# Kernel optimization log

Measured on AMD Instinct MI355X. Metric: run time of the kernel, lower is better.

The kernel has to match this reference:

```python
import jax, jax.numpy as jnp
import numpy as np

B, S, H = 8, 2048, 1024
NH, HD, NS, K = 16, 64, 64, 4  # num_heads, head_dim, state_size, conv kernel


def setup_inputs() -> dict:
    key = jax.random.key(0)
    ks = jax.random.split(key, 16)
    sc = 0.02
    return {
        "x": jax.random.normal(ks[0], (B, S, H), dtype=jnp.float32),
        # weights stored (in, out) so y = x @ W + b
        "in_proj_w": jax.random.normal(ks[1], (H, 2 * H), dtype=jnp.float32) * sc,
        "conv_w": jax.random.normal(ks[2], (H, 1, K), dtype=jnp.float32) * sc,
        "conv_b": jnp.zeros((H,), dtype=jnp.float32),
        "bb_w": jax.random.normal(ks[3], (HD, HD), dtype=jnp.float32) * sc,
        "bb_b": jnp.zeros((HD,), dtype=jnp.float32),
        "f1_w": jax.random.normal(ks[4], (HD, NS), dtype=jnp.float32) * sc,
        "f1_b": jnp.zeros((NS,), dtype=jnp.float32),
        "f2_w": jax.random.normal(ks[5], (HD, NS), dtype=jnp.float32) * sc,
        "f2_b": jnp.zeros((NS,), dtype=jnp.float32),
        "tau_a_w": jax.random.normal(ks[6], (HD, NS), dtype=jnp.float32) * sc,
        "tau_a_b": jnp.zeros((NS,), dtype=jnp.float32),
        "tau_b": jnp.zeros((NS,), dtype=jnp.float32),
        "decay_w": jax.random.normal(ks[7], (HD, NS), dtype=jnp.float32) * sc,
        "decay_b": jnp.zeros((NS,), dtype=jnp.float32),
        "state_out_w": jax.random.normal(ks[8], (NS, HD), dtype=jnp.float32) * sc,
        "state_out_b": jnp.zeros((HD,), dtype=jnp.float32),
        "out_proj_w": jax.random.normal(ks[9], (H, H), dtype=jnp.float32) * sc,
    }


def _short_conv(x, w, b):
    # x: (B,S,D) depthwise causal conv, kernel K, left-pad K-1
    xc = jnp.transpose(x, (0, 2, 1))  # (B,D,S)
    y = jax.lax.conv_general_dilated(
        xc, w, window_strides=(1,), padding=[(K - 1, 0)],
        feature_group_count=H, dimension_numbers=("NCH", "OIH", "NCH"))
    y = y + b[None, :, None]
    return jnp.transpose(y, (0, 2, 1))  # (B,S,D)


def _scan(decay, candidate):
    # decay, candidate: (B,S,NH,NS); h_t = d_t*h_{t-1} + (1-d_t)*c_t
    d = jnp.transpose(decay, (1, 0, 2, 3))      # (S,B,NH,NS)
    c = jnp.transpose(candidate, (1, 0, 2, 3))

    def step(h, dc):
        dt, ct = dc
        h = dt * h + (1.0 - dt) * ct
        return h, h

    h0 = jnp.zeros(d.shape[1:], dtype=decay.dtype)
    _, hs = jax.lax.scan(step, h0, (d, c))
    return jnp.transpose(hs, (1, 0, 2, 3))      # (B,S,NH,NS)


def reference(x, in_proj_w, conv_w, conv_b, bb_w, bb_b, f1_w, f1_b,
              f2_w, f2_b, tau_a_w, tau_a_b, tau_b, decay_w, decay_b,
              state_out_w, state_out_b, out_proj_w):
    xz = x @ in_proj_w                       # (B,S,2H)
    x_path, z_gate = jnp.split(xz, 2, axis=-1)
    x_path = jax.nn.silu(_short_conv(x_path, conv_w, conv_b))
    x_heads = x_path.reshape(B, S, NH, HD)
    bb = jax.nn.silu(x_heads @ bb_w + bb_b)  # backbone (1 layer)
    f1 = jnp.tanh(bb @ f1_w + f1_b)
    f2 = jnp.tanh(bb @ f2_w + f2_b)
    tau = jax.nn.sigmoid(bb @ tau_a_w + tau_a_b + tau_b)
    candidate = f1 * (1.0 - tau) + f2 * tau
    decay = jax.nn.sigmoid(bb @ decay_w + decay_b)
    h_seq = _scan(decay, candidate)          # (B,S,NH,NS)
    out = h_seq @ state_out_w + state_out_b  # (B,S,NH,HD)
    out = out.reshape(B, S, H)
    out = out * jax.nn.silu(z_gate)
    return out @ out_proj_w
```

## Files before the change

### kernel.cpp

```cpp
#include <hip/hip_runtime.h>
#include <hip/hip_bf16.h>
#include <math.h>

#define BN   8
#define SN   2048
#define HN   1024
#define NTOK 16384
#define NHD  16
#define HDD  64
#define NSD  64

typedef __attribute__((ext_vector_type(8))) short short8;
typedef __attribute__((ext_vector_type(4))) float f32x4;

__device__ __forceinline__ float fsig(float x)  { return 1.f / (1.f + __expf(-x)); }
__device__ __forceinline__ float fsilu(float x) { return x / (1.f + __expf(-x)); }
__device__ __forceinline__ float ftanh(float x) {
    const float t = __expf(-2.f * fabsf(x));
    const float r = (1.f - t) / (1.f + t);
    return x >= 0.f ? r : -r;
}
__device__ __forceinline__ unsigned pack_cd(float cand, float dec) {
    __hip_bfloat16 cb_ = __float2bfloat16(cand);
    __hip_bfloat16 db_ = __float2bfloat16(dec);
    return (unsigned)*(unsigned short*)&cb_ | ((unsigned)*(unsigned short*)&db_ << 16);
}
__device__ __forceinline__ void gload_lds16(const void* g, void* l) {
    __builtin_amdgcn_global_load_lds(
        (const __attribute__((address_space(1))) unsigned int*)g,
        (__attribute__((address_space(3))) unsigned int*)l, 16, 0, 0);
}

__global__ __launch_bounds__(256)
void x_to_a_bf(const float* __restrict__ X, __hip_bfloat16* __restrict__ A)
{
    const int idx = blockIdx.x * 256 + threadIdx.x;
    const int r = idx >> 7;
    const int c = idx & 127;
    const float* src = &X[(size_t)r * 1024 + c * 8];
    alignas(16) __hip_bfloat16 b[8];
#pragma unroll
    for (int j = 0; j < 8; ++j) b[j] = __float2bfloat16(src[j]);
    const int cs = (c & 120) | ((c & 7) ^ (r & 7));
    *(short8*)&A[(size_t)r * 1024 + cs * 8] = *(const short8*)b;
}

__global__ __launch_bounds__(256)
void w_to_bt_bf(const float* __restrict__ W, __hip_bfloat16* __restrict__ BT, int N)
{
    __shared__ float t[64][65];
    const int k0 = blockIdx.x * 64;
    const int n0 = blockIdx.y * 64;
    const int c  = threadIdx.x & 63, r4 = threadIdx.x >> 6;
#pragma unroll
    for (int rr = 0; rr < 64; rr += 4)
        t[rr + r4][c] = W[(size_t)(k0 + rr + r4) * N + n0 + c];
    __syncthreads();
#pragma unroll
    for (int oo = 0; oo < 2; ++oo) {
        const int o = r4 * 2 + oo;
        alignas(16) __hip_bfloat16 b[8];
#pragma unroll
        for (int j = 0; j < 8; ++j)
            b[j] = __float2bfloat16(t[o * 8 + j][c]);
        const int n = n0 + c;
        const int cglob = (k0 >> 3) + o;
        const int cs = (cglob & 120) | ((cglob & 7) ^ (n & 7));
        *(short8*)&BT[(size_t)n * 1024 + cs * 8] = *(const short8*)b;
    }
}

__global__ __launch_bounds__(256)
void w5_to_wt(const float* __restrict__ w0, const float* __restrict__ w1,
              const float* __restrict__ w2, const float* __restrict__ w3,
              const float* __restrict__ w4, __hip_bfloat16* __restrict__ WT5)
{
    const int idx = blockIdx.x * 256 + threadIdx.x;
    if (idx >= 2560) return;
    const int o = idx & 7, n = (idx >> 3) & 63, mat = idx >> 9;
    const float* W = mat == 0 ? w0 : mat == 1 ? w1 : mat == 2 ? w2 : mat == 3 ? w3 : w4;
    alignas(16) __hip_bfloat16 b[8];
#pragma unroll
    for (int j = 0; j < 8; ++j)
        b[j] = __float2bfloat16(W[(o * 8 + j) * 64 + n]);
    *(short8*)&WT5[(size_t)(mat * 64 + n) * 64 + ((o ^ (n & 7)) * 8)] = *(const short8*)b;
}

template<int NCT, int MODE>
__global__ __launch_bounds__(512, 2)
void mfma_gemm256(const __hip_bfloat16* __restrict__ A,
                  const __hip_bfloat16* __restrict__ BT,
                  float* __restrict__ out0, float* __restrict__ out1)
{
    __shared__ __hip_bfloat16 lds[2][2][16384];
    const int tid  = threadIdx.x;
    const int lane = tid & 63, wave = tid >> 6;
    const int wr   = wave >> 2, wc = wave & 3;
    const int l15  = lane & 15, l4 = lane >> 4;

    const int nwg = gridDim.x;
    const int cpx = nwg >> 3;
    const int swz = (blockIdx.x & 7) * cpx + (blockIdx.x >> 3);
    const int mt = swz / NCT, nt = swz % NCT;
    const int row0 = mt * 256, col0 = nt * 256;

    const int s_c = tid & 7;
    const int s_r = (tid >> 3) & 63;

    f32x4 acc[8][4];
#pragma unroll
    for (int m = 0; m < 8; ++m)
#pragma unroll
        for (int n = 0; n < 4; ++n) acc[m][n] = (f32x4)0.f;

#define STAGE_I(I, TT, BUF)                                                    \
    {                                                                          \
        const int mat_ = (I) >> 2;                                             \
        const int row_ = ((I) & 3) * 64 + s_r;                                 \
        const __hip_bfloat16* src_ = (mat_ == 0)                               \
            ? &A [(size_t)(row0 + row_) * 1024 + ((TT) << 6) + s_c * 8]        \
            : &BT[(size_t)(col0 + row_) * 1024 + ((TT) << 6) + s_c * 8];       \
        gload_lds16(src_, &lds[BUF][mat_][row_ * 64 + s_c * 8]);               \
    }

#pragma unroll
    for (int i = 0; i < 8; ++i) STAGE_I(i, 0, 0)
    __syncthreads();

    for (int t = 0; t < 16; ++t) {
        const int cur = t & 1, nxt = cur ^ 1;
        const bool pf = (t < 15);

#pragma unroll
        for (int ks = 0; ks < 2; ++ks) {
            if (pf) {
#pragma unroll
                for (int i = ks * 4; i < ks * 4 + 4; ++i) STAGE_I(i, t + 1, nxt)
            }

            short8 af[8], bf[4];
#pragma unroll
            for (int m = 0; m < 8; ++m) {
                const int row = wr * 128 + m * 16 + l15;
                const int ch = (ks * 4 + l4) ^ (l15 & 7);
                af[m] = *(const short8*)&lds[cur][0][row * 64 + ch * 8];
            }
#pragma unroll
            for (int n = 0; n < 4; ++n) {
                const int row = wc * 64 + n * 16 + l15;
                const int ch = (ks * 4 + l4) ^ (l15 & 7);
                bf[n] = *(const short8*)&lds[cur][1][row * 64 + ch * 8];
            }

            __builtin_amdgcn_s_setprio(1);
#pragma unroll
            for (int m = 0; m < 8; ++m)
#pragma unroll
                for (int n = 0; n < 4; ++n)
                    acc[m][n] = __builtin_amdgcn_mfma_f32_16x16x32_bf16(af[m], bf[n], acc[m][n], 0, 0, 0);
            __builtin_amdgcn_s_setprio(0);
        }
        __syncthreads();
    }
#undef STAGE_I

    const int orow = l4 * 4, ocol = l15;
#pragma unroll
    for (int M = 0; M < 8; ++M)
#pragma unroll
        for (int N = 0; N < 4; ++N) {
            const int c = col0 + wc * 64 + N * 16 + ocol;
#pragma unroll
            for (int q = 0; q < 4; ++q) {
                const int r = row0 + wr * 128 + M * 16 + orow + q;
                const float v = acc[M][N][q];
                if (MODE == 0) {
                    out0[(size_t)r * (NCT * 256) + c] = v;
                } else {
                    if (c < 1024) out0[(size_t)r * 1024 + c] = v;
                    else          out1[(size_t)r * 1024 + (c - 1024)] = fsilu(v);
                }
            }
        }
}

__global__ __launch_bounds__(256)
void conv_silu_bf(const float* __restrict__ xp, const float* __restrict__ cw,
                  const float* __restrict__ cb, __hip_bfloat16* __restrict__ Xbf)
{
    const int idx = blockIdx.x * 256 + threadIdx.x;
    const int g  = idx & 127;
    const int bt = idx >> 7;
    const int t  = bt & (SN - 1);
    const int c0 = g * 8;

    float acc[8];
#pragma unroll
    for (int j = 0; j < 8; ++j) acc[j] = cb[c0 + j];
    float4 cwv[8];
#pragma unroll
    for (int j = 0; j < 8; ++j) cwv[j] = *(const float4*)&cw[(c0 + j) * 4];
    const float* cwf = (const float*)cwv;

#pragma unroll
    for (int k = 0; k < 4; ++k) {
        if (t - 3 + k >= 0) {
            const float* xr = xp + (((size_t)(bt - 3 + k)) << 10) + c0;
            const float4 u0 = *(const float4*)&xr[0];
            const float4 u1 = *(const float4*)&xr[4];
            const float u[8] = {u0.x, u0.y, u0.z, u0.w, u1.x, u1.y, u1.z, u1.w};
#pragma unroll
            for (int j = 0; j < 8; ++j) acc[j] += cwf[j * 4 + k] * u[j];
        }
    }

    alignas(16) __hip_bfloat16 b[8];
#pragma unroll
    for (int j = 0; j < 8; ++j) b[j] = __float2bfloat16(fsilu(acc[j]));

    const int head = g >> 3;
    const int o    = g & 7;
    const size_t row = (size_t)bt * 16 + head;
    *(short8*)&Xbf[row * 64 + ((o ^ (head & 7)) * 8)] = *(const short8*)b;
}

__global__ __launch_bounds__(512, 4)
void backbone_mfma(const __hip_bfloat16* __restrict__ Xbf,
                   const __hip_bfloat16* __restrict__ WT5,
                   const float* __restrict__ bbb,
                   const float* __restrict__ f1b, const float* __restrict__ f2b,
                   const float* __restrict__ taub, const float* __restrict__ taub2,
                   const float* __restrict__ decb,
                   unsigned* __restrict__ cd)
{
    __shared__ __hip_bfloat16 Wl[5 * 64 * 64];
    __shared__ __hip_bfloat16 Bb[128 * 64];
    const int tid  = threadIdx.x;
    const int lane = tid & 63, wave = tid >> 6;
    const int l15  = lane & 15, l4 = lane >> 4;
    const int e7   = l15 & 7;

#pragma unroll
    for (int r = 0; r < 5; ++r) {
        const int blk = r * 8 + wave;
        gload_lds16(WT5 + blk * 512 + lane * 8, Wl + blk * 512);
    }

    const __hip_bfloat16* xrow = Xbf + ((size_t)(blockIdx.x * 8 + wave) * 16) * 64;
    short8 xa[2];
#pragma unroll
    for (int s = 0; s < 2; ++s)
        xa[s] = *(const short8*)&xrow[l15 * 64 + (((s * 4 + l4) ^ e7) * 8)];

    __syncthreads();

#pragma unroll
    for (int nt = 0; nt < 4; ++nt) {
        short8 wb[2];
#pragma unroll
        for (int s = 0; s < 2; ++s)
            wb[s] = *(const short8*)&Wl[(nt * 16 + l15) * 64 + (((s * 4 + l4) ^ e7) * 8)];
        f32x4 ac = (f32x4)0.f;
        ac = __builtin_amdgcn_mfma_f32_16x16x32_bf16(xa[0], wb[0], ac, 0, 0, 0);
        ac = __builtin_amdgcn_mfma_f32_16x16x32_bf16(xa[1], wb[1], ac, 0, 0, 0);
        const int col = nt * 16 + l15;
        const float bc = bbb[col];
#pragma unroll
        for (int q = 0; q < 4; ++q) {
            const int r15 = l4 * 4 + q;
            Bb[(wave * 16 + r15) * 64 + ((col >> 3) ^ (r15 & 7)) * 8 + (col & 7)] =
                __float2bfloat16(fsilu(ac[q] + bc));
        }
    }

    short8 ba[2];
#pragma unroll
    for (int s = 0; s < 2; ++s)
        ba[s] = *(const short8*)&Bb[(wave * 16 + l15) * 64 + (((s * 4 + l4) ^ e7) * 8)];

#pragma unroll
    for (int nt = 0; nt < 4; ++nt) {
        f32x4 a2[4];
#pragma unroll
        for (int m = 0; m < 4; ++m) a2[m] = (f32x4)0.f;

#pragma unroll
        for (int mat = 0; mat < 4; ++mat) {
            short8 w2[2];
#pragma unroll
            for (int s = 0; s < 2; ++s)
                w2[s] = *(const short8*)&Wl[((mat + 1) * 64 + nt * 16 + l15) * 64 + (((s * 4 + l4) ^ e7) * 8)];
            a2[mat] = __builtin_amdgcn_mfma_f32_16x16x32_bf16(ba[0], w2[0], a2[mat], 0, 0, 0);
            a2[mat] = __builtin_amdgcn_mfma_f32_16x16x32_bf16(ba[1], w2[1], a2[mat], 0, 0, 0);
        }

        const int col = nt * 16 + l15;
        const float b1 = f1b[col], b2 = f2b[col];
        const float b3 = taub[col] + taub2[col], b4 = decb[col];
        const size_t Rbase = (size_t)blockIdx.x * 128 + wave * 16;
#pragma unroll
        for (int q = 0; q < 4; ++q) {
            const size_t R = Rbase + l4 * 4 + q;
            const float f1v = ftanh(a2[0][q] + b1);
            const float f2v = ftanh(a2[1][q] + b2);
            const float tv  = fsig (a2[2][q] + b3);
            const float dv  = fsig (a2[3][q] + b4);
            cd[R * 64 + col] = pack_cd(f1v * (1.f - tv) + f2v * tv, dv);
        }
    }
}

__global__ __launch_bounds__(256)
void scan_compose(const unsigned* __restrict__ cd,
                  float* __restrict__ Ach, float* __restrict__ Bch)
{
    const int idx = blockIdx.x * 256 + threadIdx.x;
    const int p  = idx & 1023;
    const int rest = idx >> 10;
    const int ch = rest & 63, b = rest >> 6;
    float A = 1.f, Bv = 0.f;
    const size_t base = ((size_t)(b * SN + ch * 32) << 10) + p;
    for (int t = 0; t < 32; ++t) {
        const unsigned u = cd[base + ((size_t)t << 10)];
        const float c = __uint_as_float(u << 16);
        const float d = __uint_as_float(u & 0xffff0000u);
        A  *= d;
        Bv  = d * Bv + (1.f - d) * c;
    }
    Ach[(ch << 13) + (b << 10) + p] = A;
    Bch[(ch << 13) + (b << 10) + p] = Bv;
}

__global__ __launch_bounds__(256)
void scan_chunks(const float* __restrict__ Ach, const float* __restrict__ Bch,
                 float* __restrict__ hstart)
{
    const int q = blockIdx.x * 256 + threadIdx.x;
    float h = 0.f;
    for (int ch = 0; ch < 64; ++ch) {
        hstart[(ch << 13) + q] = h;
        h = Ach[(ch << 13) + q] * h + Bch[(ch << 13) + q];
    }
}

__global__ __launch_bounds__(256)
void scan_apply(const unsigned* __restrict__ cd,
                const float* __restrict__ hstart, __hip_bfloat16* __restrict__ Hhl)
{
    const int idx = blockIdx.x * 256 + threadIdx.x;
    const int p  = idx & 1023;
    const int rest = idx >> 10;
    const int ch = rest & 63, b = rest >> 6;
    const int nh = p >> 6, ns = p & 63;
    const int hpos = ((ns >> 3) ^ (nh & 7)) * 8 + (ns & 7);
    float h = hstart[(ch << 13) + (b << 10) + p];
    const int t0 = b * SN + ch * 32;
    const size_t base = ((size_t)t0 << 10) + p;
    for (int t = 0; t < 32; ++t) {
        const unsigned u = cd[base + ((size_t)t << 10)];
        const float c = __uint_as_float(u << 16);
        const float d = __uint_as_float(u & 0xffff0000u);
        h = d * h + (1.f - d) * c;
        Hhl[((size_t)(t0 + t) * 16 + nh) * 64 + hpos] = __float2bfloat16(h);
    }
}

__global__ __launch_bounds__(256, 4)
void stateout_mfma(const __hip_bfloat16* __restrict__ Hhl,
                   const float* __restrict__ sow, const float* __restrict__ sob,
                   const float* __restrict__ zs, __hip_bfloat16* __restrict__ gA)
{
    __shared__ __hip_bfloat16 Wl[64 * 64];
    __shared__ __hip_bfloat16 Hl[128 * 64];
    const int tid  = threadIdx.x;
    const int lane = tid & 63, wave = tid >> 6;
    const int l15  = lane & 15, l4 = lane >> 4;
    const int e7   = l15 & 7;

    {
        const int n = tid & 63;
        const int o0 = tid >> 6;
#pragma unroll
        for (int oo = 0; oo < 2; ++oo) {
            const int o = o0 + oo * 4;
            alignas(16) __hip_bfloat16 b[8];
#pragma unroll
            for (int j = 0; j < 8; ++j)
                b[j] = __float2bfloat16(sow[(o * 8 + j) * 64 + n]);
            *(short8*)&Wl[n * 64 + ((o ^ (n & 7)) * 8)] = *(const short8*)b;
        }
    }
    const __hip_bfloat16* hsrc = Hhl + (size_t)blockIdx.x * 8192;
#pragma unroll
    for (int r = 0; r < 4; ++r) {
        const int blk = r * 4 + wave;
        gload_lds16(hsrc + blk * 512 + lane * 8, Hl + blk * 512);
    }
    __syncthreads();

    short8 ha[2][2];
#pragma unroll
    for (int mt2 = 0; mt2 < 2; ++mt2)
#pragma unroll
        for (int s = 0; s < 2; ++s)
            ha[mt2][s] = *(const short8*)&Hl[(wave * 32 + mt2 * 16 + l15) * 64 + (((s * 4 + l4) ^ e7) * 8)];

#pragma unroll
    for (int nt = 0; nt < 4; ++nt) {
        short8 wb[2];
#pragma unroll
        for (int s = 0; s < 2; ++s)
            wb[s] = *(const short8*)&Wl[(nt * 16 + l15) * 64 + (((s * 4 + l4) ^ e7) * 8)];
        f32x4 ac[2] = {(f32x4)0.f, (f32x4)0.f};
#pragma unroll
        for (int mt2 = 0; mt2 < 2; ++mt2) {
            ac[mt2] = __builtin_amdgcn_mfma_f32_16x16x32_bf16(ha[mt2][0], wb[0], ac[mt2], 0, 0, 0);
            ac[mt2] = __builtin_amdgcn_mfma_f32_16x16x32_bf16(ha[mt2][1], wb[1], ac[mt2], 0, 0, 0);
        }
        const int col = nt * 16 + l15;
        const float bj = sob[col];
#pragma unroll
        for (int mt2 = 0; mt2 < 2; ++mt2)
#pragma unroll
            for (int q = 0; q < 4; ++q) {
                const size_t th = (size_t)blockIdx.x * 128 + wave * 32 + mt2 * 16 + l4 * 4 + q;
                const float v = (ac[mt2][q] + bj) * zs[th * 64 + col];
                const size_t token = th >> 4;
                const int colg = (int)(th & 15) * 64 + col;
                const int cg = colg >> 3, jg = colg & 7;
                const int cs = (cg & 120) | ((cg & 7) ^ ((int)(token & 7)));
                gA[token * 1024 + cs * 8 + jg] = __float2bfloat16(v);
            }
    }
}

extern "C" void kernel_launch(void* const* d_in, const int* in_sizes, int n_in,
                              void* d_out, int out_size, void* d_ws, size_t ws_size,
                              hipStream_t stream)
{
    const float* x     = (const float*)d_in[0];
    const float* ipw   = (const float*)d_in[1];
    const float* cw    = (const float*)d_in[2];
    const float* cb    = (const float*)d_in[3];
    const float* bbw   = (const float*)d_in[4];
    const float* bbb   = (const float*)d_in[5];
    const float* f1w   = (const float*)d_in[6];
    const float* f1b   = (const float*)d_in[7];
    const float* f2w   = (const float*)d_in[8];
    const float* f2b   = (const float*)d_in[9];
    const float* tauw  = (const float*)d_in[10];
    const float* taub  = (const float*)d_in[11];
    const float* taub2 = (const float*)d_in[12];
    const float* decw  = (const float*)d_in[13];
    const float* decb  = (const float*)d_in[14];
    const float* sow   = (const float*)d_in[15];
    const float* sob   = (const float*)d_in[16];
    const float* opw   = (const float*)d_in[17];

    float* out = (float*)d_out;
    char*  ws  = (char*)d_ws;
    const size_t MB = 1024 * 1024;

    __hip_bfloat16* Abf   = (__hip_bfloat16*)(ws);
    __hip_bfloat16* Xbf   = (__hip_bfloat16*)(ws);
    __hip_bfloat16* Hhl   = (__hip_bfloat16*)(ws + 32 * MB);
    float*          xpath = (float*)(ws + 64 * MB);
    __hip_bfloat16* gA    = (__hip_bfloat16*)(ws + 64 * MB);
    __hip_bfloat16* BTin  = (__hip_bfloat16*)(ws + 128 * MB);
    unsigned*       cd    = (unsigned*)(ws + 128 * MB);
    __hip_bfloat16* WT5   = (__hip_bfloat16*)(ws + 192 * MB);
    float*          Ach   = (float*)(ws + 192 * MB);
    float*          Bch   = Ach + 524288;
    float*          hst   = Bch + 524288;
    __hip_bfloat16* BTout = (__hip_bfloat16*)(ws + 192 * MB);
    float*          zsilu = out;

    x_to_a_bf<<<8192, 256, 0, stream>>>(x, Abf);
    w_to_bt_bf<<<dim3(16, 32), 256, 0, stream>>>(ipw, BTin, 2048);
    w5_to_wt<<<10, 256, 0, stream>>>(bbw, f1w, f2w, tauw, decw, WT5);
    mfma_gemm256<8, 1><<<512, 512, 0, stream>>>(Abf, BTin, xpath, zsilu);
    conv_silu_bf<<<8192, 256, 0, stream>>>(xpath, cw, cb, Xbf);
    backbone_mfma<<<2048, 512, 0, stream>>>(Xbf, WT5, bbb, f1b, f2b,
                                            taub, taub2, decb, cd);
    scan_compose<<<2048, 256, 0, stream>>>(cd, Ach, Bch);
    scan_chunks<<<32, 256, 0, stream>>>(Ach, Bch, hst);
    scan_apply<<<2048, 256, 0, stream>>>(cd, hst, Hhl);
    w_to_bt_bf<<<dim3(16, 16), 256, 0, stream>>>(opw, BTout, 1024);
    stateout_mfma<<<2048, 256, 0, stream>>>(Hhl, sow, sob, zsilu, gA);
    mfma_gemm256<4, 0><<<256, 512, 0, stream>>>(gA, BTout, out, nullptr);
}
```

Measured before the change: 320.8 us.

## Shrink GEMM tiles to 128x256 with BK=32 and emit bf16 intermediates

Reworks the MFMA GEMM to use 128x256 output tiles with a 32-wide K step, a smaller LDS footprint and a 4-block occupancy hint, doubling the grid. The swizzle pattern in the A/B staging kernels and in stateout changes from 8-chunk to 4-chunk XOR to match. The input projection now writes x_path and silu(z) as bf16 instead of fp32, and the conv and stateout kernels read bf16. The goal is more occupancy and less intermediate memory traffic, at the cost of lower per-tile reuse, more barriers per K, and reduced precision in the intermediates.

```diff
diff --git a/kernel.cpp b/kernel.cpp
--- a/kernel.cpp
+++ b/kernel.cpp
@@ -25,6 +25,9 @@
     __hip_bfloat16 db_ = __float2bfloat16(dec);
     return (unsigned)*(unsigned short*)&cb_ | ((unsigned)*(unsigned short*)&db_ << 16);
 }
+__device__ __forceinline__ float bf2f(unsigned short u) {
+    return __uint_as_float((unsigned)u << 16);
+}
 __device__ __forceinline__ void gload_lds16(const void* g, void* l) {
     __builtin_amdgcn_global_load_lds(
         (const __attribute__((address_space(1))) unsigned int*)g,
@@ -41,7 +44,7 @@
     alignas(16) __hip_bfloat16 b[8];
 #pragma unroll
     for (int j = 0; j < 8; ++j) b[j] = __float2bfloat16(src[j]);
-    const int cs = (c & 120) | ((c & 7) ^ (r & 7));
+    const int cs = (c & ~3) | ((c & 3) ^ (r & 3));
     *(short8*)&A[(size_t)r * 1024 + cs * 8] = *(const short8*)b;
 }
 
@@ -65,7 +68,7 @@
             b[j] = __float2bfloat16(t[o * 8 + j][c]);
         const int n = n0 + c;
         const int cglob = (k0 >> 3) + o;
-        const int cs = (cglob & 120) | ((cglob & 7) ^ (n & 7));
+        const int cs = (cglob & ~3) | ((cglob & 3) ^ (n & 3));
         *(short8*)&BT[(size_t)n * 1024 + cs * 8] = *(const short8*)b;
     }
 }
@@ -87,12 +90,13 @@
 }
 
 template<int NCT, int MODE>
-__global__ __launch_bounds__(512, 2)
-void mfma_gemm256(const __hip_bfloat16* __restrict__ A,
-                  const __hip_bfloat16* __restrict__ BT,
-                  float* __restrict__ out0, float* __restrict__ out1)
-{
-    __shared__ __hip_bfloat16 lds[2][2][16384];
+__global__ __launch_bounds__(512, 4)
+void mfma_gemm(const __hip_bfloat16* __restrict__ A,
+               const __hip_bfloat16* __restrict__ BT,
+               float* __restrict__ outf,
+               __hip_bfloat16* __restrict__ xb, __hip_bfloat16* __restrict__ zb)
+{
+    __shared__ __hip_bfloat16 lds[2][12288];
     const int tid  = threadIdx.x;
     const int lane = tid & 63, wave = tid >> 6;
     const int wr   = wave >> 2, wc = wave & 3;
@@ -102,90 +106,83 @@
     const int cpx = nwg >> 3;
     const int swz = (blockIdx.x & 7) * cpx + (blockIdx.x >> 3);
     const int mt = swz / NCT, nt = swz % NCT;
-    const int row0 = mt * 256, col0 = nt * 256;
-
-    const int s_c = tid & 7;
-    const int s_r = (tid >> 3) & 63;
-
-    f32x4 acc[8][4];
-#pragma unroll
-    for (int m = 0; m < 8; ++m)
+    const int row0 = mt * 128, col0 = nt * 256;
+
+    const int s_c = tid & 3;
+    const int s_r = tid >> 2;
+
+    f32x4 acc[4][4];
+#pragma unroll
+    for (int m = 0; m < 4; ++m)
 #pragma unroll
         for (int n = 0; n < 4; ++n) acc[m][n] = (f32x4)0.f;
 
-#define STAGE_I(I, TT, BUF)                                                    \
+    const int rdch = (0 ^ 0);
+
+#define STAGE(TT, BUF)                                                         \
     {                                                                          \
-        const int mat_ = (I) >> 2;                                             \
-        const int row_ = ((I) & 3) * 64 + s_r;                                 \
-        const __hip_bfloat16* src_ = (mat_ == 0)                               \
-            ? &A [(size_t)(row0 + row_) * 1024 + ((TT) << 6) + s_c * 8]        \
-            : &BT[(size_t)(col0 + row_) * 1024 + ((TT) << 6) + s_c * 8];       \
-        gload_lds16(src_, &lds[BUF][mat_][row_ * 64 + s_c * 8]);               \
-    }
-
-#pragma unroll
-    for (int i = 0; i < 8; ++i) STAGE_I(i, 0, 0)
+        const int kk_ = (TT) << 5;                                             \
+        gload_lds16(&A[(size_t)(row0 + s_r) * 1024 + kk_ + s_c * 8],           \
+                    &lds[BUF][s_r * 32 + s_c * 8]);                            \
+        _Pragma("unroll")                                                      \
+        for (int h_ = 0; h_ < 2; ++h_) {                                       \
+            const int r_ = h_ * 128 + s_r;                                     \
+            gload_lds16(&BT[(size_t)(col0 + r_) * 1024 + kk_ + s_c * 8],       \
+                        &lds[BUF][4096 + r_ * 32 + s_c * 8]);                  \
+        }                                                                      \
+    }
+
+    STAGE(0, 0)
     __syncthreads();
 
-    for (int t = 0; t < 16; ++t) {
+    for (int t = 0; t < 32; ++t) {
         const int cur = t & 1, nxt = cur ^ 1;
-        const bool pf = (t < 15);
-
-#pragma unroll
-        for (int ks = 0; ks < 2; ++ks) {
-            if (pf) {
-#pragma unroll
-                for (int i = ks * 4; i < ks * 4 + 4; ++i) STAGE_I(i, t + 1, nxt)
-            }
-
-            short8 af[8], bf[4];
-#pragma unroll
-            for (int m = 0; m < 8; ++m) {
-                const int row = wr * 128 + m * 16 + l15;
-                const int ch = (ks * 4 + l4) ^ (l15 & 7);
-                af[m] = *(const short8*)&lds[cur][0][row * 64 + ch * 8];
-            }
-#pragma unroll
-            for (int n = 0; n < 4; ++n) {
-                const int row = wc * 64 + n * 16 + l15;
-                const int ch = (ks * 4 + l4) ^ (l15 & 7);
-                bf[n] = *(const short8*)&lds[cur][1][row * 64 + ch * 8];
-            }
-
-            __builtin_amdgcn_s_setprio(1);
-#pragma unroll
-            for (int m = 0; m < 8; ++m)
-#pragma unroll
-                for (int n = 0; n < 4; ++n)
-                    acc[m][n] = __builtin_amdgcn_mfma_f32_16x16x32_bf16(af[m], bf[n], acc[m][n], 0, 0, 0);
-            __builtin_amdgcn_s_setprio(0);
-        }
+        if (t < 31) STAGE(t + 1, nxt)
+
+        const int ch = (l4 ^ (l15 & 3)) * 8;
+        short8 af[4], bf[4];
+#pragma unroll
+        for (int m = 0; m < 4; ++m)
+            af[m] = *(const short8*)&lds[cur][(wr * 64 + m * 16 + l15) * 32 + ch];
+#pragma unroll
+        for (int n = 0; n < 4; ++n)
+            bf[n] = *(const short8*)&lds[cur][4096 + (wc * 64 + n * 16 + l15) * 32 + ch];
+
+        __builtin_amdgcn_s_setprio(1);
+#pragma unroll
+        for (int m = 0; m < 4; ++m)
+#pragma unroll
+            for (int n = 0; n < 4; ++n)
+                acc[m][n] = __builtin_amdgcn_mfma_f32_16x16x32_bf16(af[m], bf[n], acc[m][n], 0, 0, 0);
+        __builtin_amdgcn_s_setprio(0);
+
         __syncthreads();
     }
-#undef STAGE_I
+#undef STAGE
 
     const int orow = l4 * 4, ocol = l15;
 #pragma unroll
-    for (int M = 0; M < 8; ++M)
-#pragma unroll
-        for (int N = 0; N < 4; ++N) {
-            const int c = col0 + wc * 64 + N * 16 + ocol;
+    for (int m = 0; m < 4; ++m)
+#pragma unroll
+        for (int n = 0; n < 4; ++n) {
+            const int c = col0 + wc * 64 + n * 16 + ocol;
 #pragma unroll
             for (int q = 0; q < 4; ++q) {
-                const int r = row0 + wr * 128 + M * 16 + orow + q;
-                const float v = acc[M][N][q];
+                const int r = row0 + wr * 64 + m * 16 + orow + q;
+                const float v = acc[m][n][q];
                 if (MODE == 0) {
-                    out0[(size_t)r * (NCT * 256) + c] = v;
+                    outf[(size_t)r * (NCT * 256) + c] = v;
                 } else {
-                    if (c < 1024) out0[(size_t)r * 1024 + c] = v;
-                    else          out1[(size_t)r * 1024 + (c - 1024)] = fsilu(v);
+                    if (c < 1024) xb[(size_t)r * 1024 + c] = __float2bfloat16(v);
+                    else          zb[(size_t)r * 1024 + (c - 1024)] = __float2bfloat16(fsilu(v));
                 }
             }
         }
-}
-
-__global__ __launch_bounds__(256)
-void conv_silu_bf(const float* __restrict__ xp, const float* __restrict__ cw,
+    (void)rdch;
+}
+
+__global__ __launch_bounds__(256)
+void conv_silu_bf(const __hip_bfloat16* __restrict__ xp, const float* __restrict__ cw,
                   const float* __restrict__ cb, __hip_bfloat16* __restrict__ Xbf)
 {
     const int idx = blockIdx.x * 256 + threadIdx.x;
@@ -205,12 +202,10 @@
 #pragma unroll
     for (int k = 0; k < 4; ++k) {
         if (t - 3 + k >= 0) {
-            const float* xr = xp + (((size_t)(bt - 3 + k)) << 10) + c0;
-            const float4 u0 = *(const float4*)&xr[0];
-            const float4 u1 = *(const float4*)&xr[4];
-            const float u[8] = {u0.x, u0.y, u0.z, u0.w, u1.x, u1.y, u1.z, u1.w};
-#pragma unroll
-            for (int j = 0; j < 8; ++j) acc[j] += cwf[j * 4 + k] * u[j];
+            const short8 u = *(const short8*)&xp[(((size_t)(bt - 3 + k)) << 10) + c0];
+#pragma unroll
+            for (int j = 0; j < 8; ++j)
+                acc[j] += cwf[j * 4 + k] * bf2f((unsigned short)u[j]);
         }
     }
 
@@ -368,7 +363,7 @@
 __global__ __launch_bounds__(256, 4)
 void stateout_mfma(const __hip_bfloat16* __restrict__ Hhl,
                    const float* __restrict__ sow, const float* __restrict__ sob,
-                   const float* __restrict__ zs, __hip_bfloat16* __restrict__ gA)
+                   const __hip_bfloat16* __restrict__ zs, __hip_bfloat16* __restrict__ gA)
 {
     __shared__ __hip_bfloat16 Wl[64 * 64];
     __shared__ __hip_bfloat16 Hl[128 * 64];
@@ -424,11 +419,12 @@
 #pragma unroll
             for (int q = 0; q < 4; ++q) {
                 const size_t th = (size_t)blockIdx.x * 128 + wave * 32 + mt2 * 16 + l4 * 4 + q;
-                const float v = (ac[mt2][q] + bj) * zs[th * 64 + col];
+                const float z = bf2f(*(const unsigned short*)&zs[th * 64 + col]);
+                const float v = (ac[mt2][q] + bj) * z;
                 const size_t token = th >> 4;
                 const int colg = (int)(th & 15) * 64 + col;
                 const int cg = colg >> 3, jg = colg & 7;
-                const int cs = (cg & 120) | ((cg & 7) ^ ((int)(token & 7)));
+                const int cs = (cg & ~3) | ((cg & 3) ^ ((int)(token & 3)));
                 gA[token * 1024 + cs * 8 + jg] = __float2bfloat16(v);
             }
     }
@@ -444,8 +440,8 @@
     const float* cb    = (const float*)d_in[3];
     const float* bbw   = (const float*)d_in[4];
     const float* bbb   = (const float*)d_in[5];
+    const float* f1b_  = (const float*)d_in[7];
     const float* f1w   = (const float*)d_in[6];
-    const float* f1b   = (const float*)d_in[7];
     const float* f2w   = (const float*)d_in[8];
     const float* f2b   = (const float*)d_in[9];
     const float* tauw  = (const float*)d_in[10];
@@ -464,7 +460,7 @@
     __hip_bfloat16* Abf   = (__hip_bfloat16*)(ws);
     __hip_bfloat16* Xbf   = (__hip_bfloat16*)(ws);
     __hip_bfloat16* Hhl   = (__hip_bfloat16*)(ws + 32 * MB);
-    float*          xpath = (float*)(ws + 64 * MB);
+    __hip_bfloat16* xpath = (__hip_bfloat16*)(ws + 64 * MB);
     __hip_bfloat16* gA    = (__hip_bfloat16*)(ws + 64 * MB);
     __hip_bfloat16* BTin  = (__hip_bfloat16*)(ws + 128 * MB);
     unsigned*       cd    = (unsigned*)(ws + 128 * MB);
@@ -473,19 +469,19 @@
     float*          Bch   = Ach + 524288;
     float*          hst   = Bch + 524288;
     __hip_bfloat16* BTout = (__hip_bfloat16*)(ws + 192 * MB);
-    float*          zsilu = out;
+    __hip_bfloat16* zsilu = (__hip_bfloat16*)out;
 
     x_to_a_bf<<<8192, 256, 0, stream>>>(x, Abf);
     w_to_bt_bf<<<dim3(16, 32), 256, 0, stream>>>(ipw, BTin, 2048);
     w5_to_wt<<<10, 256, 0, stream>>>(bbw, f1w, f2w, tauw, decw, WT5);
-    mfma_gemm256<8, 1><<<512, 512, 0, stream>>>(Abf, BTin, xpath, zsilu);
+    mfma_gemm<8, 1><<<1024, 512, 0, stream>>>(Abf, BTin, nullptr, xpath, zsilu);
     conv_silu_bf<<<8192, 256, 0, stream>>>(xpath, cw, cb, Xbf);
-    backbone_mfma<<<2048, 512, 0, stream>>>(Xbf, WT5, bbb, f1b, f2b,
+    backbone_mfma<<<2048, 512, 0, stream>>>(Xbf, WT5, bbb, f1b_, f2b,
                                             taub, taub2, decb, cd);
     scan_compose<<<2048, 256, 0, stream>>>(cd, Ach, Bch);
     scan_chunks<<<32, 256, 0, stream>>>(Ach, Bch, hst);
     scan_apply<<<2048, 256, 0, stream>>>(cd, hst, Hhl);
     w_to_bt_bf<<<dim3(16, 16), 256, 0, stream>>>(opw, BTout, 1024);
     stateout_mfma<<<2048, 256, 0, stream>>>(Hhl, sow, sob, zsilu, gA);
-    mfma_gemm256<4, 0><<<256, 512, 0, stream>>>(gA, BTout, out, nullptr);
-}
+    mfma_gemm<4, 0><<<512, 512, 0, stream>>>(gA, BTout, out, nullptr, nullptr);
+}
```

New measurement: 315.6 us. About the same (-1.6%).
